# Kernel tuning notes

Measured on AMD Instinct MI355X. Metric: run time of the kernel, lower is better.

Reference implementation:

```python
import jax, jax.numpy as jnp
import numpy as np

B, S, D = 1, 2048, 2048
H, KVH = 32, 8
HD = D // H          # 64
N_REP = H // KVH     # 4
ROPE_THETA = 10000.0
NEG = -1e9


def setup_inputs() -> dict:
    key = jax.random.key(0)
    ks = jax.random.split(key, 8)
    x = jax.random.normal(ks[0], (B, S, D), dtype=jnp.float32)
    # RoPE tables: freqs_cis[t, j] = exp(i * t * theta^{-2j/HD}), j in [0, HD/2)
    inv_freq = 1.0 / (ROPE_THETA ** (jnp.arange(0, HD, 2, dtype=jnp.float32) / HD))
    angles = jnp.arange(S, dtype=jnp.float32)[:, None] * inv_freq[None, :]  # (S, HD/2)
    freqs_cos = jnp.cos(angles)
    freqs_sin = jnp.sin(angles)
    # causal additive mask (S, S)
    mask = jnp.where(jnp.tril(jnp.ones((S, S), dtype=bool)), 0.0, NEG).astype(jnp.float32)
    sc = 0.02
    wq = jax.random.normal(ks[1], (D, H * HD), dtype=jnp.float32) * sc
    wk = jax.random.normal(ks[2], (D, KVH * HD), dtype=jnp.float32) * sc
    wv = jax.random.normal(ks[3], (D, KVH * HD), dtype=jnp.float32) * sc
    wo = jax.random.normal(ks[4], (H * HD, D), dtype=jnp.float32) * sc
    fw = jax.random.normal(ks[5], (HD, HD), dtype=jnp.float32) * sc
    fb = jnp.zeros((HD,), dtype=jnp.float32)
    return {"x": x, "freqs_cos": freqs_cos, "freqs_sin": freqs_sin, "mask": mask,
            "wq": wq, "wk": wk, "wv": wv, "wo": wo, "fw": fw, "fb": fb,
            "start_pos": 0}


def _rope(t, cos, sin):
    # t: (B, S, h, HD) -> complex rotate pairs along last dim
    tr = t.reshape(*t.shape[:-1], HD // 2, 2)
    c = cos[None, :, None, :]  # (1, S, 1, HD/2)
    s = sin[None, :, None, :]
    re = tr[..., 0] * c - tr[..., 1] * s
    im = tr[..., 0] * s + tr[..., 1] * c
    return jnp.stack([re, im], axis=-1).reshape(t.shape)


def reference(x, freqs_cos, freqs_sin, mask, wq, wk, wv, wo, fw, fb, start_pos):
    b, s, _ = x.shape
    xq = (x @ wq).reshape(b, s, H, HD)
    xk = (x @ wk).reshape(b, s, KVH, HD)
    xv = (x @ wv).reshape(b, s, KVH, HD)
    xq = _rope(xq, freqs_cos, freqs_sin)
    xk = _rope(xk, freqs_cos, freqs_sin)
    # GQA: repeat kv heads (repeat_interleave on head dim)
    keys = jnp.repeat(xk, N_REP, axis=2)    # (b, s, H, HD)
    values = jnp.repeat(xv, N_REP, axis=2)
    q = xq.transpose(0, 2, 1, 3)            # (b, H, s, HD)
    k = keys.transpose(0, 2, 1, 3)
    v = values.transpose(0, 2, 1, 3)
    scores = jnp.einsum("bhqd,bhkd->bhqk", q, k) / np.sqrt(HD).astype(np.float32)
    scores = scores + mask[None, None, :, :]
    probs = jax.nn.softmax(scores.astype(jnp.float32), axis=-1).astype(q.dtype)
    out = jnp.einsum("bhqk,bhkd->bhqd", probs, v)  # (b, H, s, HD)
    # shared per-head FFN: Linear(HD, HD) + SiLU, vectorized over heads
    out = jax.nn.silu(out @ fw + fb)
    out = out.transpose(0, 2, 1, 3).reshape(b, s, H * HD)
    return out @ wo
```

## Files before the change

kernel.cpp:

```cpp
#include <hip/hip_runtime.h>
#include <stdint.h>

#define S_LEN 2048
#define DMODEL 2048
#define NH 32
#define NKV 8
#define HD 64

typedef __attribute__((ext_vector_type(8))) __bf16 bf16x8;
typedef __attribute__((ext_vector_type(4))) float f32x4;
typedef __attribute__((ext_vector_type(16))) float f32x16;

__device__ __forceinline__ unsigned short f2bf(float f) {
    union { float f; uint32_t u; } v; v.f = f;
    uint32_t u = v.u;
    u += 0x7FFFu + ((u >> 16) & 1u);
    return (unsigned short)(u >> 16);
}

__device__ __forceinline__ uint32_t cvt_pk_bf16(float lo, float hi) {
    uint32_t r;
    asm("v_cvt_pk_bf16_f32 %0, %1, %2" : "=v"(r) : "v"(lo), "v"(hi));
    return r;
}

#define GLDS16(g, l)                                                          \
    __builtin_amdgcn_global_load_lds(                                         \
        (const __attribute__((address_space(1))) unsigned int*)(g),           \
        (__attribute__((address_space(3))) unsigned int*)(l), 16, 0, 0)

__device__ const int kUQT[24] = {15,15,7,14,14,13,13,6,12,12,11,11,5,10,10,9,9,4,8,8,3,2,1,0};
__device__ const int kUCH[24] = {0,1,0,0,1,0,1,0,0,1,0,1,0,0,1,0,1,0,0,1,0,0,0,0};
__device__ const int kUSP[24] = {1,1,0,1,1,1,1,0,1,1,1,1,0,1,1,1,1,0,1,1,0,0,0,0};

__global__ void cast_bf16_kernel(const float* __restrict__ src,
                                 unsigned short* __restrict__ dst, int n) {
    int g = (blockIdx.x * blockDim.x + threadIdx.x) * 8;
    if (g >= n) return;
    float4 a = *(const float4*)&src[g];
    float4 b = *(const float4*)&src[g + 4];
    unsigned short o[8];
    o[0] = f2bf(a.x); o[1] = f2bf(a.y); o[2] = f2bf(a.z); o[3] = f2bf(a.w);
    o[4] = f2bf(b.x); o[5] = f2bf(b.y); o[6] = f2bf(b.z); o[7] = f2bf(b.w);
    *(uint4*)&dst[g] = *(const uint4*)o;
}

__global__ void transpose_cast_kernel(const float* __restrict__ src,
                                      unsigned short* __restrict__ dst,
                                      int R, int C) {
    __shared__ float tile[32][33];
    int c0 = blockIdx.x * 32, r0 = blockIdx.y * 32;
    int tx = threadIdx.x, ty = threadIdx.y;
#pragma unroll
    for (int i = 0; i < 32; i += 8)
        tile[ty + i][tx] = src[(size_t)(r0 + ty + i) * C + c0 + tx];
    __syncthreads();
#pragma unroll
    for (int i = 0; i < 32; i += 8)
        dst[(size_t)(c0 + ty + i) * R + r0 + tx] = f2bf(tile[tx][ty + i]);
}

__global__ __launch_bounds__(256) void gemm_bt_kernel(
    const unsigned short* __restrict__ A, const unsigned short* __restrict__ BT,
    float* __restrict__ C0, float* __restrict__ C1, int M, int N,
    int Kstride, int Klen) {
    __shared__ unsigned short As[2][128 * 32];
    __shared__ unsigned short Bs[2][128 * 32];
    const int t = threadIdx.x;
    const int lane = t & 63, wave = t >> 6;
    const int wr = wave >> 1, wc = wave & 1;
    const int m0 = blockIdx.x * 128, n0 = blockIdx.y * 128;
    const int koff = blockIdx.z * Klen;
    float* __restrict__ C = blockIdx.z ? C1 : C0;
    const int l15 = lane & 15, lhi = lane >> 4;
    f32x4 acc[4][4] = {};
    const unsigned short* ga = A + (size_t)(m0 + (t >> 2)) * Kstride + koff + (t & 3) * 8;
    const unsigned short* gb = BT + (size_t)(n0 + (t >> 2)) * Kstride + koff + (t & 3) * 8;

    GLDS16(ga, &As[0][t * 8]);
    GLDS16(ga + (size_t)64 * Kstride, &As[0][t * 8 + 64 * 32]);
    GLDS16(gb, &Bs[0][t * 8]);
    GLDS16(gb + (size_t)64 * Kstride, &Bs[0][t * 8 + 64 * 32]);
    __syncthreads();

    int cur = 0;
    for (int k0 = 0; k0 < Klen; k0 += 32) {
        if (k0 + 32 < Klen) {
            GLDS16(ga + k0 + 32, &As[cur ^ 1][t * 8]);
            GLDS16(ga + (size_t)64 * Kstride + k0 + 32, &As[cur ^ 1][t * 8 + 64 * 32]);
            GLDS16(gb + k0 + 32, &Bs[cur ^ 1][t * 8]);
            GLDS16(gb + (size_t)64 * Kstride + k0 + 32, &Bs[cur ^ 1][t * 8 + 64 * 32]);
        }
        bf16x8 af[4], bfr[4];
#pragma unroll
        for (int m = 0; m < 4; m++)
            af[m] = *(const bf16x8*)&As[cur][(wr * 64 + m * 16 + l15) * 32 + lhi * 8];
#pragma unroll
        for (int n = 0; n < 4; n++)
            bfr[n] = *(const bf16x8*)&Bs[cur][(wc * 64 + n * 16 + l15) * 32 + lhi * 8];
#pragma unroll
        for (int m = 0; m < 4; m++)
#pragma unroll
            for (int n = 0; n < 4; n++)
                acc[m][n] = __builtin_amdgcn_mfma_f32_16x16x32_bf16(
                    af[m], bfr[n], acc[m][n], 0, 0, 0);
        __syncthreads();
        cur ^= 1;
    }
#pragma unroll
    for (int m = 0; m < 4; m++) {
        int row = m0 + wr * 64 + m * 16 + lhi * 4;
#pragma unroll
        for (int n = 0; n < 4; n++) {
            int col = n0 + wc * 64 + n * 16 + l15;
#pragma unroll
            for (int r = 0; r < 4; r++)
                C[(size_t)(row + r) * N + col] = acc[m][n][r];
        }
    }
}

__global__ void add_f32_kernel(float* __restrict__ out,
                               const float* __restrict__ p1, int n4) {
    int g = blockIdx.x * blockDim.x + threadIdx.x;
    if (g >= n4) return;
    float4 a = *(const float4*)&out[g * 4];
    float4 b = *(const float4*)&p1[g * 4];
    a.x += b.x; a.y += b.y; a.z += b.z; a.w += b.w;
    *(float4*)&out[g * 4] = a;
}

__global__ void rope_q_kernel(const float* __restrict__ Cqkv,
                              const float* __restrict__ cb,
                              const float* __restrict__ sb,
                              unsigned short* __restrict__ Q) {
    const float CS = 0.125f * 1.44269504f;
    int g = blockIdx.x * 256 + threadIdx.x;
    int i = g & 31;
    int h = (g >> 5) & 31;
    int s = g >> 10;
    float2 v = *(const float2*)&Cqkv[(size_t)s * 3072 + h * 64 + 2 * i];
    float cc = cb[s * 32 + i], ss = sb[s * 32 + i];
    ushort2 o;
    o.x = f2bf((v.x * cc - v.y * ss) * CS);
    o.y = f2bf((v.x * ss + v.y * cc) * CS);
    *(ushort2*)&Q[(size_t)h * (S_LEN * HD) + s * HD + 2 * i] = o;
}

__global__ void rope_k_kernel(const float* __restrict__ Cqkv,
                              const float* __restrict__ cb,
                              const float* __restrict__ sb,
                              unsigned short* __restrict__ Kb) {
    int g = blockIdx.x * 256 + threadIdx.x;
    int i = g & 31;
    int kvh = (g >> 5) & 7;
    int s = g >> 8;
    float2 v = *(const float2*)&Cqkv[(size_t)s * 3072 + 2048 + kvh * 64 + 2 * i];
    float cc = cb[s * 32 + i], ss = sb[s * 32 + i];
    ushort2 o;
    o.x = f2bf(v.x * cc - v.y * ss);
    o.y = f2bf(v.x * ss + v.y * cc);
    *(ushort2*)&Kb[(size_t)kvh * (S_LEN * HD) + s * HD + 2 * i] = o;
}

__global__ void v_transpose_kernel(const float* __restrict__ Cqkv,
                                   unsigned short* __restrict__ VT) {
    __shared__ float tile[32][33];
    int kvh = blockIdx.z;
    int d0 = blockIdx.x * 32, s0 = blockIdx.y * 32;
    int tx = threadIdx.x, ty = threadIdx.y;
#pragma unroll
    for (int i = 0; i < 32; i += 8)
        tile[ty + i][tx] =
            Cqkv[(size_t)(s0 + ty + i) * 3072 + 2560 + kvh * 64 + d0 + tx];
    __syncthreads();
#pragma unroll
    for (int i = 0; i < 32; i += 8)
        VT[(size_t)kvh * (HD * S_LEN) + (size_t)(d0 + ty + i) * S_LEN + s0 + tx] =
            f2bf(tile[tx][ty + i]);
}

__global__ __launch_bounds__(256) void flash_kernel(
    const unsigned short* __restrict__ Q, const unsigned short* __restrict__ Kg,
    const unsigned short* __restrict__ VTg, unsigned short* __restrict__ O,
    float* __restrict__ Opart, float* __restrict__ ML) {
    __shared__ unsigned short Ks[3][4096];
    __shared__ unsigned short Vs[3][4096];
    const int t = threadIdx.x, lane = t & 63, wave = t >> 6;
    const int l31 = lane & 31, hi = lane >> 5;
    const int bid = blockIdx.x;
    const int h = bid & 31, u = bid >> 5;
    const int qt = kUQT[u], ch = kUCH[u], sp = kUSP[u];
    const int kvh = h >> 2;

    const int kt0 = sp ? ch * (qt + 1) : 0;
    const int ktN = sp ? kt0 + qt + 1 : 2 * qt + 2;

    const int srow = t >> 3;
    const int scol = ((t & 7) * 8) ^ ((srow & 7) * 8);
    const unsigned short* gk = Kg + ((size_t)kvh * S_LEN + srow) * HD + scol;
    const unsigned short* gv = VTg + ((size_t)kvh * HD + srow) * S_LEN + scol;

    const int q0 = qt * 128;
    const int qw0 = q0 + wave * 32;
    const int q = qw0 + l31;

    const unsigned short* qp = Q + ((size_t)h * S_LEN + q) * HD + hi * 8;
    bf16x8 qf0 = *(const bf16x8*)(qp);
    bf16x8 qf1 = *(const bf16x8*)(qp + 16);
    bf16x8 qf2 = *(const bf16x8*)(qp + 32);
    bf16x8 qf3 = *(const bf16x8*)(qp + 48);

    f32x16 oacc0 = {}, oacc1 = {};
    float mrun = -1e30f, lrun = 0.f;

    {
        const size_t kva = (size_t)kt0 * 64, kvb = kva + 64;
        GLDS16(gk + kva * HD, &Ks[0][t * 8]);
        GLDS16(gk + (kva + 32) * HD, &Ks[0][t * 8 + 2048]);
        GLDS16(gv + kva, &Vs[0][t * 8]);
        GLDS16(gv + (size_t)32 * S_LEN + kva, &Vs[0][t * 8 + 2048]);
        GLDS16(gk + kvb * HD, &Ks[1][t * 8]);
        GLDS16(gk + (kvb + 32) * HD, &Ks[1][t * 8 + 2048]);
        GLDS16(gv + kvb, &Vs[1][t * 8]);
        GLDS16(gv + (size_t)32 * S_LEN + kvb, &Vs[1][t * 8 + 2048]);
    }

    int cb = 0, pfb = 2;
#pragma unroll 1
    for (int kt = kt0; kt < ktN; ++kt) {
        if (kt + 1 < ktN) asm volatile("s_waitcnt vmcnt(4)" ::: "memory");
        else              asm volatile("s_waitcnt vmcnt(0)" ::: "memory");
        __builtin_amdgcn_s_barrier();
        __builtin_amdgcn_sched_barrier(0);
        if (kt + 2 < ktN) {
            const size_t kvp = (size_t)(kt + 2) * 64;
            GLDS16(gk + kvp * HD, &Ks[pfb][t * 8]);
            GLDS16(gk + (kvp + 32) * HD, &Ks[pfb][t * 8 + 2048]);
            GLDS16(gv + kvp, &Vs[pfb][t * 8]);
            GLDS16(gv + (size_t)32 * S_LEN + kvp, &Vs[pfb][t * 8 + 2048]);
        }
        pfb = (pfb == 2) ? 0 : pfb + 1;
        const int kv0 = kt * 64;
        const int mycb = cb;
        cb = (cb == 2) ? 0 : cb + 1;
        if (kv0 > qw0 + 31) continue;
        const unsigned short* ksb = Ks[mycb];
        const unsigned short* vsb = Vs[mycb];
        const int sw = (l31 & 7) * 8;
        f32x16 s0 = {}, s1 = {};
#pragma unroll
        for (int kc = 0; kc < 4; kc++) {
            bf16x8 k0 = *(const bf16x8*)&ksb[l31 * 64 + ((16 * kc + 8 * hi) ^ sw)];
            bf16x8 k1 = *(const bf16x8*)&ksb[(32 + l31) * 64 + ((16 * kc + 8 * hi) ^ sw)];
            bf16x8 qc = (kc == 0) ? qf0 : (kc == 1) ? qf1 : (kc == 2) ? qf2 : qf3;
            s0 = __builtin_amdgcn_mfma_f32_32x32x16_bf16(k0, qc, s0, 0, 0, 0);
            s1 = __builtin_amdgcn_mfma_f32_32x32x16_bf16(k1, qc, s1, 0, 0, 0);
        }
        float p0[16], p1[16];
        if (kv0 + 63 <= qw0) {
#pragma unroll
            for (int r = 0; r < 16; r++) { p0[r] = s0[r]; p1[r] = s1[r]; }
        } else {
#pragma unroll
            for (int r = 0; r < 16; r++) {
                int rr = (r & 3) + 8 * (r >> 2) + 4 * hi;
                p0[r] = (kv0 + rr <= q) ? s0[r] : -1e30f;
                p1[r] = (kv0 + 32 + rr <= q) ? s1[r] : -1e30f;
            }
        }
        float t8[8];
#pragma unroll
        for (int r = 0; r < 8; r++)
            t8[r] = fmaxf(fmaxf(p0[r], p0[r + 8]), fmaxf(p1[r], p1[r + 8]));
        float lm = fmaxf(fmaxf(fmaxf(t8[0], t8[4]), fmaxf(t8[1], t8[5])),
                         fmaxf(fmaxf(t8[2], t8[6]), fmaxf(t8[3], t8[7])));
        if (!__all(lm - mrun <= 8.f)) {
            float rm = fmaxf(lm, __shfl_xor(lm, 32));
            float mnew = fmaxf(mrun, rm);
            float sc = exp2f(mrun - mnew);
            mrun = mnew;
            lrun *= sc;
            oacc0 *= sc;
            oacc1 *= sc;
        }
#pragma unroll
        for (int r = 0; r < 16; r++) {
            p0[r] = exp2f(p0[r] - mrun);
            p1[r] = exp2f(p1[r] - mrun);
        }
        float sA = 0.f, sB = 0.f, sC = 0.f, sD = 0.f;
#pragma unroll
        for (int r = 0; r < 4; r++) {
            sA += p0[r] + p1[r];
            sB += p0[r + 4] + p1[r + 4];
            sC += p0[r + 8] + p1[r + 8];
            sD += p0[r + 12] + p1[r + 12];
        }
        lrun += (sA + sB) + (sC + sD);
        bf16x8 pf[4];
#pragma unroll
        for (int kc = 0; kc < 4; kc++) {
            const int sub = (kc & 1) * 8;
            uint32_t Wl0, Wl1, Wh0, Wh1;
            if (kc < 2) {
                Wl0 = cvt_pk_bf16(p0[sub + 0], p0[sub + 1]);
                Wl1 = cvt_pk_bf16(p0[sub + 2], p0[sub + 3]);
                Wh0 = cvt_pk_bf16(p0[sub + 4], p0[sub + 5]);
                Wh1 = cvt_pk_bf16(p0[sub + 6], p0[sub + 7]);
            } else {
                Wl0 = cvt_pk_bf16(p1[sub + 0], p1[sub + 1]);
                Wl1 = cvt_pk_bf16(p1[sub + 2], p1[sub + 3]);
                Wh0 = cvt_pk_bf16(p1[sub + 4], p1[sub + 5]);
                Wh1 = cvt_pk_bf16(p1[sub + 6], p1[sub + 7]);
            }
            uint32_t sw0 = hi ? Wl0 : Wh0, sw1 = hi ? Wl1 : Wh1;
            uint32_t rc0 = __shfl_xor((int)sw0, 32);
            uint32_t rc1 = __shfl_xor((int)sw1, 32);
            uint32_t kp0 = hi ? Wh0 : Wl0, kp1 = hi ? Wh1 : Wl1;
            uint32_t F0 = hi ? rc0 : kp0;
            uint32_t F1 = hi ? rc1 : kp1;
            uint32_t F2 = hi ? kp0 : rc0;
            uint32_t F3 = hi ? kp1 : rc1;
            uint4 fu = {F0, F1, F2, F3};
            pf[kc] = *(const bf16x8*)&fu;
        }
#pragma unroll
        for (int kc = 0; kc < 4; kc++) {
            bf16x8 v0 = *(const bf16x8*)&vsb[l31 * 64 + ((16 * kc + 8 * hi) ^ sw)];
            bf16x8 v1 = *(const bf16x8*)&vsb[(32 + l31) * 64 + ((16 * kc + 8 * hi) ^ sw)];
            oacc0 = __builtin_amdgcn_mfma_f32_32x32x16_bf16(v0, pf[kc], oacc0, 0, 0, 0);
            oacc1 = __builtin_amdgcn_mfma_f32_32x32x16_bf16(v1, pf[kc], oacc1, 0, 0, 0);
        }
    }
    lrun += __shfl_xor(lrun, 32);
    const int qrow = wave * 32 + l31;
    if (sp) {
        const int pidx = (h * 8 + (qt - 8)) * 2 + ch;
        float* po = Opart + ((size_t)pidx * 128 + qrow) * 64 + 4 * hi;
#pragma unroll
        for (int g = 0; g < 4; g++) {
            float4 a = {oacc0[4 * g], oacc0[4 * g + 1], oacc0[4 * g + 2], oacc0[4 * g + 3]};
            *(float4*)(po + 8 * g) = a;
            float4 b = {oacc1[4 * g], oacc1[4 * g + 1], oacc1[4 * g + 2], oacc1[4 * g + 3]};
            *(float4*)(po + 32 + 8 * g) = b;
        }
        if (hi == 0) {
            ML[((size_t)pidx * 128 + qrow) * 2] = mrun;
            ML[((size_t)pidx * 128 + qrow) * 2 + 1] = lrun;
        }
    } else {
        float rinv = 1.f / lrun;
        unsigned short* ob = O + ((size_t)h * S_LEN + q) * HD + 4 * hi;
#pragma unroll
        for (int g = 0; g < 4; g++) {
            uint32_t a0 = cvt_pk_bf16(oacc0[4 * g] * rinv, oacc0[4 * g + 1] * rinv);
            uint32_t a1 = cvt_pk_bf16(oacc0[4 * g + 2] * rinv, oacc0[4 * g + 3] * rinv);
            uint2 u0 = {a0, a1};
            *(uint2*)(ob + 8 * g) = u0;
            uint32_t b0 = cvt_pk_bf16(oacc1[4 * g] * rinv, oacc1[4 * g + 1] * rinv);
            uint32_t b1 = cvt_pk_bf16(oacc1[4 * g + 2] * rinv, oacc1[4 * g + 3] * rinv);
            uint2 u1 = {b0, b1};
            *(uint2*)(ob + 32 + 8 * g) = u1;
        }
    }
}

__global__ __launch_bounds__(256) void flash_combine_kernel(
    const float* __restrict__ Opart, const float* __restrict__ ML,
    unsigned short* __restrict__ attn) {
    const int bid = blockIdx.x;
    const int h = bid & 31, j = bid >> 5;
    const int qt = 8 + j;
    const int t = threadIdx.x;
    const int qrow = t >> 1, d0 = (t & 1) * 32;
    const int base = (h * 8 + j) * 2;
    const float mA = ML[((size_t)base * 128 + qrow) * 2];
    const float lA = ML[((size_t)base * 128 + qrow) * 2 + 1];
    const float mB = ML[((size_t)(base + 1) * 128 + qrow) * 2];
    const float lB = ML[((size_t)(base + 1) * 128 + qrow) * 2 + 1];
    const float m = fmaxf(mA, mB);
    const float wA = exp2f(mA - m), wB = exp2f(mB - m);
    const float rinv = 1.f / (lA * wA + lB * wB);
    const float* pA = Opart + ((size_t)base * 128 + qrow) * 64 + d0;
    const float* pB = Opart + ((size_t)(base + 1) * 128 + qrow) * 64 + d0;
    unsigned short* po = attn + ((size_t)h * S_LEN + qt * 128 + qrow) * HD + d0;
#pragma unroll
    for (int dd = 0; dd < 32; dd += 8) {
        float4 a0 = *(const float4*)&pA[dd], a1 = *(const float4*)&pA[dd + 4];
        float4 b0 = *(const float4*)&pB[dd], b1 = *(const float4*)&pB[dd + 4];
        unsigned short o[8];
        o[0] = f2bf((a0.x * wA + b0.x * wB) * rinv);
        o[1] = f2bf((a0.y * wA + b0.y * wB) * rinv);
        o[2] = f2bf((a0.z * wA + b0.z * wB) * rinv);
        o[3] = f2bf((a0.w * wA + b0.w * wB) * rinv);
        o[4] = f2bf((a1.x * wA + b1.x * wB) * rinv);
        o[5] = f2bf((a1.y * wA + b1.y * wB) * rinv);
        o[6] = f2bf((a1.z * wA + b1.z * wB) * rinv);
        o[7] = f2bf((a1.w * wA + b1.w * wB) * rinv);
        *(uint4*)&po[dd] = *(const uint4*)o;
    }
}

__global__ __launch_bounds__(256) void fw_silu_kernel(
    const unsigned short* __restrict__ AT, const unsigned short* __restrict__ fwT,
    const float* __restrict__ fb, unsigned short* __restrict__ h2) {
    const int t = threadIdx.x, lane = t & 63, wave = t >> 6;
    const int l15 = lane & 15, lhi = lane >> 4;
    const int r0 = blockIdx.x * 64 + wave * 16;
    const unsigned short* ap = AT + (size_t)(r0 + l15) * HD + lhi * 8;
    bf16x8 a0 = *(const bf16x8*)ap;
    bf16x8 a1 = *(const bf16x8*)(ap + 32);
    f32x4 acc[4] = {};
#pragma unroll
    for (int nb = 0; nb < 4; nb++) {
        const unsigned short* bp = fwT + (size_t)(nb * 16 + l15) * HD + lhi * 8;
        bf16x8 b0 = *(const bf16x8*)bp;
        bf16x8 b1 = *(const bf16x8*)(bp + 32);
        acc[nb] = __builtin_amdgcn_mfma_f32_16x16x32_bf16(a0, b0, acc[nb], 0, 0, 0);
        acc[nb] = __builtin_amdgcn_mfma_f32_16x16x32_bf16(a1, b1, acc[nb], 0, 0, 0);
    }
#pragma unroll
    for (int nb = 0; nb < 4; nb++) {
        int col = nb * 16 + l15;
        float bias = fb[col];
#pragma unroll
        for (int r = 0; r < 4; r++) {
            int row = r0 + lhi * 4 + r;
            int s = row & (S_LEN - 1), hh = row >> 11;
            float x = acc[nb][r] + bias;
            float sg = 1.f / (1.f + exp2f(-x * 1.44269504f));
            h2[(size_t)s * DMODEL + hh * HD + col] = f2bf(x * sg);
        }
    }
}

extern "C" void kernel_launch(void* const* d_in, const int* in_sizes, int n_in,
                              void* d_out, int out_size, void* d_ws, size_t ws_size,
                              hipStream_t stream) {
    const float* x = (const float*)d_in[0];
    const float* fcos = (const float*)d_in[1];
    const float* fsin = (const float*)d_in[2];
    const float* wq = (const float*)d_in[4];
    const float* wk = (const float*)d_in[5];
    const float* wv = (const float*)d_in[6];
    const float* wo = (const float*)d_in[7];
    const float* fw = (const float*)d_in[8];
    const float* fb = (const float*)d_in[9];
    float* out = (float*)d_out;

    char* ws = (char*)d_ws;
    size_t off = 0;
    auto alloc = [&](size_t bytes) {
        void* p = ws + off;
        off += (bytes + 255) & ~(size_t)255;
        return p;
    };
    unsigned short* wqkvT = (unsigned short*)alloc((size_t)3072 * 2048 * 2);
    unsigned short* woT   = (unsigned short*)alloc((size_t)2048 * 2048 * 2);
    unsigned short* fwT   = (unsigned short*)alloc((size_t)64 * 64 * 2);
    float*          Cqkv  = (float*)alloc((size_t)2048 * 3072 * 4);
    unsigned short* Qb    = (unsigned short*)alloc((size_t)NH * S_LEN * HD * 2);
    unsigned short* Kb    = (unsigned short*)alloc((size_t)NKV * S_LEN * HD * 2);
    unsigned short* VT    = (unsigned short*)alloc((size_t)NKV * HD * S_LEN * 2);
    unsigned short* xb    = (unsigned short*)alloc((size_t)2048 * 2048 * 2);
    float*          ML    = (float*)alloc((size_t)512 * 128 * 2 * 4);
    unsigned short* attn = (unsigned short*)Cqkv;
    float* P1 = (float*)((char*)Cqkv + (size_t)NH * S_LEN * HD * 2);
    float* Opart = P1;
    unsigned short* h2 = xb;

    dim3 tb(32, 8);
    cast_bf16_kernel<<<2048, 256, 0, stream>>>(x, xb, 2048 * 2048);
    transpose_cast_kernel<<<dim3(64, 64), tb, 0, stream>>>(wq, wqkvT, 2048, 2048);
    transpose_cast_kernel<<<dim3(16, 64), tb, 0, stream>>>(wk, wqkvT + (size_t)2048 * 2048, 2048, 512);
    transpose_cast_kernel<<<dim3(16, 64), tb, 0, stream>>>(wv, wqkvT + (size_t)2560 * 2048, 2048, 512);
    transpose_cast_kernel<<<dim3(64, 64), tb, 0, stream>>>(wo, woT, 2048, 2048);
    transpose_cast_kernel<<<dim3(2, 2), tb, 0, stream>>>(fw, fwT, 64, 64);

    gemm_bt_kernel<<<dim3(16, 24, 1), 256, 0, stream>>>(xb, wqkvT, Cqkv, nullptr,
                                                        2048, 3072, 2048, 2048);

    rope_q_kernel<<<8192, 256, 0, stream>>>(Cqkv, fcos, fsin, Qb);
    rope_k_kernel<<<2048, 256, 0, stream>>>(Cqkv, fcos, fsin, Kb);
    v_transpose_kernel<<<dim3(2, 64, 8), tb, 0, stream>>>(Cqkv, VT);

    flash_kernel<<<768, 256, 0, stream>>>(Qb, Kb, VT, attn, Opart, ML);
    flash_combine_kernel<<<256, 256, 0, stream>>>(Opart, ML, attn);

    fw_silu_kernel<<<1024, 256, 0, stream>>>(attn, fwT, fb, h2);

    gemm_bt_kernel<<<dim3(16, 16, 2), 256, 0, stream>>>(h2, woT, out, P1,
                                                        2048, 2048, 2048, 1024);
    add_f32_kernel<<<4096, 256, 0, stream>>>(out, P1, 1048576);
}
```

Baseline: 193.1 us.

## Triple-buffer GEMM loads, swizzle workgroups, emit bf16 QKV output

The GEMM moves from a double-buffered to a triple-buffered global-to-LDS pipeline, waiting with explicit vmcnt so only one barrier is needed per K step. Workgroup IDs are remapped with an XCD-style swizzle so neighbouring tiles share L2. The QKV projection now writes bf16 instead of fp32, which halves the write traffic and the reads in the rope and V-transpose kernels. The extra rounding of Q, K and V to bf16 before RoPE adds a little error, and attn and P1 now get their own workspace buffers instead of aliasing Cqkv.

```diff
diff --git a/kernel.cpp b/kernel.cpp
--- a/kernel.cpp
+++ b/kernel.cpp
@@ -16,6 +16,12 @@
     uint32_t u = v.u;
     u += 0x7FFFu + ((u >> 16) & 1u);
     return (unsigned short)(u >> 16);
+}
+
+__device__ __forceinline__ float bf2f(unsigned short b) {
+    union { uint32_t u; float f; } v;
+    v.u = ((uint32_t)b) << 16;
+    return v.f;
 }
 
 __device__ __forceinline__ uint32_t cvt_pk_bf16(float lo, float hi) {
@@ -60,62 +66,82 @@
         dst[(size_t)(c0 + ty + i) * R + r0 + tx] = f2bf(tile[tx][ty + i]);
 }
 
+template <bool BF16OUT>
 __global__ __launch_bounds__(256) void gemm_bt_kernel(
     const unsigned short* __restrict__ A, const unsigned short* __restrict__ BT,
-    float* __restrict__ C0, float* __restrict__ C1, int M, int N,
-    int Kstride, int Klen) {
-    __shared__ unsigned short As[2][128 * 32];
-    __shared__ unsigned short Bs[2][128 * 32];
+    float* __restrict__ C0, float* __restrict__ C1,
+    unsigned short* __restrict__ Cb, int M, int N, int Kstride, int Klen) {
+    __shared__ unsigned short As[3][128 * 32];
+    __shared__ unsigned short Bs[3][128 * 32];
     const int t = threadIdx.x;
     const int lane = t & 63, wave = t >> 6;
     const int wr = wave >> 1, wc = wave & 1;
-    const int m0 = blockIdx.x * 128, n0 = blockIdx.y * 128;
+    const int gx = gridDim.x;
+    const int nwg = gx * gridDim.y;
+    const int wg = blockIdx.y * gx + blockIdx.x;
+    const int swz = (wg & 7) * (nwg >> 3) + (wg >> 3);
+    const int m0 = (swz % gx) * 128, n0 = (swz / gx) * 128;
     const int koff = blockIdx.z * Klen;
-    float* __restrict__ C = blockIdx.z ? C1 : C0;
     const int l15 = lane & 15, lhi = lane >> 4;
     f32x4 acc[4][4] = {};
     const unsigned short* ga = A + (size_t)(m0 + (t >> 2)) * Kstride + koff + (t & 3) * 8;
     const unsigned short* gb = BT + (size_t)(n0 + (t >> 2)) * Kstride + koff + (t & 3) * 8;
-
-    GLDS16(ga, &As[0][t * 8]);
-    GLDS16(ga + (size_t)64 * Kstride, &As[0][t * 8 + 64 * 32]);
-    GLDS16(gb, &Bs[0][t * 8]);
-    GLDS16(gb + (size_t)64 * Kstride, &Bs[0][t * 8 + 64 * 32]);
-    __syncthreads();
-
-    int cur = 0;
-    for (int k0 = 0; k0 < Klen; k0 += 32) {
-        if (k0 + 32 < Klen) {
-            GLDS16(ga + k0 + 32, &As[cur ^ 1][t * 8]);
-            GLDS16(ga + (size_t)64 * Kstride + k0 + 32, &As[cur ^ 1][t * 8 + 64 * 32]);
-            GLDS16(gb + k0 + 32, &Bs[cur ^ 1][t * 8]);
-            GLDS16(gb + (size_t)64 * Kstride + k0 + 32, &Bs[cur ^ 1][t * 8 + 64 * 32]);
-        }
+    const int nk = Klen >> 5;
+
+#define GSTAGE(buf, kt)                                                       \
+    {                                                                         \
+        const int k0_ = (kt) * 32;                                            \
+        GLDS16(ga + k0_, &As[buf][t * 8]);                                    \
+        GLDS16(ga + (size_t)64 * Kstride + k0_, &As[buf][t * 8 + 64 * 32]);   \
+        GLDS16(gb + k0_, &Bs[buf][t * 8]);                                    \
+        GLDS16(gb + (size_t)64 * Kstride + k0_, &Bs[buf][t * 8 + 64 * 32]);   \
+    }
+
+    GSTAGE(0, 0);
+    GSTAGE(1, 1);
+
+    int cb = 0, pfb = 2;
+#pragma unroll 1
+    for (int kt = 0; kt < nk; ++kt) {
+        if (kt + 1 < nk) asm volatile("s_waitcnt vmcnt(4)" ::: "memory");
+        else             asm volatile("s_waitcnt vmcnt(0)" ::: "memory");
+        __builtin_amdgcn_s_barrier();
+        __builtin_amdgcn_sched_barrier(0);
+        if (kt + 2 < nk) GSTAGE(pfb, kt + 2);
+        pfb = (pfb == 2) ? 0 : pfb + 1;
+        const int mycb = cb;
+        cb = (cb == 2) ? 0 : cb + 1;
         bf16x8 af[4], bfr[4];
 #pragma unroll
         for (int m = 0; m < 4; m++)
-            af[m] = *(const bf16x8*)&As[cur][(wr * 64 + m * 16 + l15) * 32 + lhi * 8];
+            af[m] = *(const bf16x8*)&As[mycb][(wr * 64 + m * 16 + l15) * 32 + lhi * 8];
 #pragma unroll
         for (int n = 0; n < 4; n++)
-            bfr[n] = *(const bf16x8*)&Bs[cur][(wc * 64 + n * 16 + l15) * 32 + lhi * 8];
+            bfr[n] = *(const bf16x8*)&Bs[mycb][(wc * 64 + n * 16 + l15) * 32 + lhi * 8];
 #pragma unroll
         for (int m = 0; m < 4; m++)
 #pragma unroll
             for (int n = 0; n < 4; n++)
                 acc[m][n] = __builtin_amdgcn_mfma_f32_16x16x32_bf16(
                     af[m], bfr[n], acc[m][n], 0, 0, 0);
-        __syncthreads();
-        cur ^= 1;
-    }
+    }
+#undef GSTAGE
 #pragma unroll
     for (int m = 0; m < 4; m++) {
         int row = m0 + wr * 64 + m * 16 + lhi * 4;
 #pragma unroll
         for (int n = 0; n < 4; n++) {
             int col = n0 + wc * 64 + n * 16 + l15;
-#pragma unroll
-            for (int r = 0; r < 4; r++)
-                C[(size_t)(row + r) * N + col] = acc[m][n][r];
+            if (BF16OUT) {
+#pragma unroll
+                for (int r = 0; r < 4; r++)
+                    Cb[(size_t)(row + r) * N + col] = f2bf(acc[m][n][r]);
+            } else {
+                float* __restrict__ C = blockIdx.z ? C1 : C0;
+#pragma unroll
+                for (int r = 0; r < 4; r++)
+                    C[(size_t)(row + r) * N + col] = acc[m][n][r];
+            }
         }
     }
 }
@@ -130,7 +156,7 @@
     *(float4*)&out[g * 4] = a;
 }
 
-__global__ void rope_q_kernel(const float* __restrict__ Cqkv,
+__global__ void rope_q_kernel(const unsigned short* __restrict__ Cqkv,
                               const float* __restrict__ cb,
                               const float* __restrict__ sb,
                               unsigned short* __restrict__ Q) {
@@ -139,15 +165,16 @@
     int i = g & 31;
     int h = (g >> 5) & 31;
     int s = g >> 10;
-    float2 v = *(const float2*)&Cqkv[(size_t)s * 3072 + h * 64 + 2 * i];
+    ushort2 v = *(const ushort2*)&Cqkv[(size_t)s * 3072 + h * 64 + 2 * i];
+    float vx = bf2f(v.x), vy = bf2f(v.y);
     float cc = cb[s * 32 + i], ss = sb[s * 32 + i];
     ushort2 o;
-    o.x = f2bf((v.x * cc - v.y * ss) * CS);
-    o.y = f2bf((v.x * ss + v.y * cc) * CS);
+    o.x = f2bf((vx * cc - vy * ss) * CS);
+    o.y = f2bf((vx * ss + vy * cc) * CS);
     *(ushort2*)&Q[(size_t)h * (S_LEN * HD) + s * HD + 2 * i] = o;
 }
 
-__global__ void rope_k_kernel(const float* __restrict__ Cqkv,
+__global__ void rope_k_kernel(const unsigned short* __restrict__ Cqkv,
                               const float* __restrict__ cb,
                               const float* __restrict__ sb,
                               unsigned short* __restrict__ Kb) {
@@ -155,17 +182,18 @@
     int i = g & 31;
     int kvh = (g >> 5) & 7;
     int s = g >> 8;
-    float2 v = *(const float2*)&Cqkv[(size_t)s * 3072 + 2048 + kvh * 64 + 2 * i];
+    ushort2 v = *(const ushort2*)&Cqkv[(size_t)s * 3072 + 2048 + kvh * 64 + 2 * i];
+    float vx = bf2f(v.x), vy = bf2f(v.y);
     float cc = cb[s * 32 + i], ss = sb[s * 32 + i];
     ushort2 o;
-    o.x = f2bf(v.x * cc - v.y * ss);
-    o.y = f2bf(v.x * ss + v.y * cc);
+    o.x = f2bf(vx * cc - vy * ss);
+    o.y = f2bf(vx * ss + vy * cc);
     *(ushort2*)&Kb[(size_t)kvh * (S_LEN * HD) + s * HD + 2 * i] = o;
 }
 
-__global__ void v_transpose_kernel(const float* __restrict__ Cqkv,
+__global__ void v_transpose_kernel(const unsigned short* __restrict__ Cqkv,
                                    unsigned short* __restrict__ VT) {
-    __shared__ float tile[32][33];
+    __shared__ unsigned short tile[32][33];
     int kvh = blockIdx.z;
     int d0 = blockIdx.x * 32, s0 = blockIdx.y * 32;
     int tx = threadIdx.x, ty = threadIdx.y;
@@ -177,7 +205,7 @@
 #pragma unroll
     for (int i = 0; i < 32; i += 8)
         VT[(size_t)kvh * (HD * S_LEN) + (size_t)(d0 + ty + i) * S_LEN + s0 + tx] =
-            f2bf(tile[tx][ty + i]);
+            tile[tx][ty + i];
 }
 
 __global__ __launch_bounds__(256) void flash_kernel(
@@ -459,14 +487,14 @@
     unsigned short* wqkvT = (unsigned short*)alloc((size_t)3072 * 2048 * 2);
     unsigned short* woT   = (unsigned short*)alloc((size_t)2048 * 2048 * 2);
     unsigned short* fwT   = (unsigned short*)alloc((size_t)64 * 64 * 2);
-    float*          Cqkv  = (float*)alloc((size_t)2048 * 3072 * 4);
+    unsigned short* Cqkv  = (unsigned short*)alloc((size_t)2048 * 3072 * 2);
     unsigned short* Qb    = (unsigned short*)alloc((size_t)NH * S_LEN * HD * 2);
     unsigned short* Kb    = (unsigned short*)alloc((size_t)NKV * S_LEN * HD * 2);
     unsigned short* VT    = (unsigned short*)alloc((size_t)NKV * HD * S_LEN * 2);
     unsigned short* xb    = (unsigned short*)alloc((size_t)2048 * 2048 * 2);
     float*          ML    = (float*)alloc((size_t)512 * 128 * 2 * 4);
-    unsigned short* attn = (unsigned short*)Cqkv;
-    float* P1 = (float*)((char*)Cqkv + (size_t)NH * S_LEN * HD * 2);
+    unsigned short* attn  = (unsigned short*)alloc((size_t)NH * S_LEN * HD * 2);
+    float*          P1    = (float*)alloc((size_t)2048 * 2048 * 4);
     float* Opart = P1;
     unsigned short* h2 = xb;
 
@@ -478,8 +506,8 @@
     transpose_cast_kernel<<<dim3(64, 64), tb, 0, stream>>>(wo, woT, 2048, 2048);
     transpose_cast_kernel<<<dim3(2, 2), tb, 0, stream>>>(fw, fwT, 64, 64);
 
-    gemm_bt_kernel<<<dim3(16, 24, 1), 256, 0, stream>>>(xb, wqkvT, Cqkv, nullptr,
-                                                        2048, 3072, 2048, 2048);
+    gemm_bt_kernel<true><<<dim3(16, 24, 1), 256, 0, stream>>>(
+        xb, wqkvT, nullptr, nullptr, Cqkv, 2048, 3072, 2048, 2048);
 
     rope_q_kernel<<<8192, 256, 0, stream>>>(Cqkv, fcos, fsin, Qb);
     rope_k_kernel<<<2048, 256, 0, stream>>>(Cqkv, fcos, fsin, Kb);
@@ -490,7 +518,7 @@
 
     fw_silu_kernel<<<1024, 256, 0, stream>>>(attn, fwT, fb, h2);
 
-    gemm_bt_kernel<<<dim3(16, 16, 2), 256, 0, stream>>>(h2, woT, out, P1,
-                                                        2048, 2048, 2048, 1024);
+    gemm_bt_kernel<false><<<dim3(16, 16, 2), 256, 0, stream>>>(
+        h2, woT, out, P1, nullptr, 2048, 2048, 2048, 1024);
     add_f32_kernel<<<4096, 256, 0, stream>>>(out, P1, 1048576);
 }
```

Result: no change. 189.4 us (-1.9%).
